# Kernel tuning notes

Measured on AMD Instinct MI355X. Metric: run time of the kernel, lower is better.

The kernel has to match this reference:

```python
import jax, jax.numpy as jnp
import numpy as np

B, H, L, N = 16, 256, 4096, 64
N2 = N // 2  # conjugate-pair parameterization: keep half the state modes


def setup_inputs() -> dict:
    key = jax.random.key(0)
    ks = jax.random.split(key, 12)
    x = jax.random.normal(ks[0], (B, H, L), jnp.float32)
    # BatchNorm1d params + running stats (inference mode)
    g1 = jnp.ones((H,), jnp.float32); b1 = jnp.zeros((H,), jnp.float32)
    m1 = 0.1 * jax.random.normal(ks[1], (H,), jnp.float32)
    v1 = 1.0 + 0.1 * jax.random.uniform(ks[2], (H,), jnp.float32)
    g2 = jnp.ones((H,), jnp.float32); b2 = jnp.zeros((H,), jnp.float32)
    m2 = 0.1 * jax.random.normal(ks[3], (H,), jnp.float32)
    v2 = 1.0 + 0.1 * jax.random.uniform(ks[4], (H,), jnp.float32)
    # S4 SSM kernel parameters (S4D-Lin init); bidirectional -> 2 channels of C
    log_dt = jnp.log(1e-3) + (jnp.log(1e-1) - jnp.log(1e-3)) * jax.random.uniform(ks[5], (H,), jnp.float32)
    logA_re = jnp.log(0.5) * jnp.ones((H, N2), jnp.float32)  # A_real = -exp(logA_re) = -0.5
    A_im = jnp.pi * jnp.broadcast_to(jnp.arange(N2, dtype=jnp.float32), (H, N2))
    C_re = jax.random.normal(ks[6], (2, H, N2), jnp.float32) * np.float32(0.5 ** 0.5)
    C_im = jax.random.normal(ks[7], (2, H, N2), jnp.float32) * np.float32(0.5 ** 0.5)
    D = jax.random.normal(ks[8], (H,), jnp.float32)  # skip term
    # S4 output linear: Conv1d(H, 2H, 1) followed by GLU
    Wo = jax.random.normal(ks[9], (2 * H, H), jnp.float32) / np.float32(np.sqrt(H))
    bo = jnp.zeros((2 * H,), jnp.float32)
    # FFN 1x1 convs
    W2 = jax.random.normal(ks[10], (2 * H, H), jnp.float32) / np.float32(np.sqrt(H))
    b2f = jnp.zeros((2 * H,), jnp.float32)
    W3 = jax.random.normal(ks[11], (H, 2 * H), jnp.float32) / np.float32(np.sqrt(2 * H))
    b3 = jnp.zeros((H,), jnp.float32)
    return dict(x=x, g1=g1, b1=b1, m1=m1, v1=v1, log_dt=log_dt, logA_re=logA_re,
                A_im=A_im, C_re=C_re, C_im=C_im, D=D, Wo=Wo, bo=bo,
                g2=g2, b2=b2, m2=m2, v2=v2, W2=W2, b2f=b2f, W3=W3, b3=b3)


def _bn(x, g, b, m, v, eps=1e-5):
    # inference-mode BatchNorm1d over channel dim of (B, H, L)
    scale = g / jnp.sqrt(v + eps)
    return (x - m[:, None]) * scale[:, None] + b[:, None]


def _s4(x, log_dt, logA_re, A_im, C_re, C_im, D, Wo, bo):
    # x: (B, H, L). Bidirectional diagonal SSM via FFT convolution.
    Ln = x.shape[-1]
    Hh = x.shape[1]
    dt = jnp.exp(log_dt)                               # (H,)
    A = -jnp.exp(logA_re) + 1j * A_im                  # (H, N2)
    dtA = dt[:, None] * A                              # (H, N2)
    C = (C_re + 1j * C_im) * (jnp.exp(dtA) - 1.0) / A  # (2, H, N2) ZOH discretization
    vand = jnp.exp(dtA[:, :, None] * jnp.arange(Ln))   # (H, N2, L) Vandermonde
    k = 2.0 * jnp.einsum('chn,hnl->chl', C, vand).real  # (2, H, L) fwd/bwd kernels
    k_fwd, k_bwd = k[0], k[1]
    zpad = jnp.zeros_like(k_fwd)
    k_full = (jnp.concatenate([k_fwd, zpad], axis=-1)
              + jnp.concatenate([zpad, k_bwd[:, ::-1]], axis=-1))  # (H, 2L)
    u_f = jnp.fft.rfft(x, n=2 * Ln)
    k_f = jnp.fft.rfft(k_full, n=2 * Ln)
    y = jnp.fft.irfft(u_f * k_f, n=2 * Ln)[..., :Ln]   # (B, H, L)
    y = y + D[:, None] * x                             # skip connection
    y = jax.nn.gelu(y, approximate=False)
    z = jnp.einsum('oi,bil->bol', Wo, y) + bo[:, None]  # (B, 2H, L)
    return z[:, :Hh] * jax.nn.sigmoid(z[:, Hh:])        # GLU -> (B, H, L)


def reference(x, g1, b1, m1, v1, log_dt, logA_re, A_im, C_re, C_im, D, Wo, bo,
              g2, b2, m2, v2, W2, b2f, W3, b3):
    # residual 1: BN -> S4 -> add
    res = x
    h = _bn(x, g1, b1, m1, v1)
    h = _s4(h, log_dt, logA_re, A_im, C_re, C_im, D, Wo, bo)
    x = res + h
    # residual 2: BN -> conv1x1(H->2H) -> GELU -> conv1x1(2H->H) -> add
    res = x
    h = _bn(x, g2, b2, m2, v2)
    h = jnp.einsum('oi,bil->bol', W2, h) + b2f[:, None]
    h = jax.nn.gelu(h, approximate=False)
    h = jnp.einsum('oi,bil->bol', W3, h) + b3[:, None]
    return res + h
```

## Files before the change

kernel.cpp:

```cpp
#include <hip/hip_runtime.h>

#define BB 16
#define HH 256
#define LL 4096
#define NN2 32

using f32x16 = __attribute__((ext_vector_type(16))) float;
using bfx8   = __attribute__((ext_vector_type(8))) short;

static constexpr float BN_EPS = 1e-5f;

__device__ __forceinline__ float gelu_exact(float v) {
    return 0.5f * v * (1.0f + erff(v * 0.70710678118654752f));
}
__device__ __forceinline__ float sigmoidf_(float v) {
    return 1.0f / (1.0f + expf(-v));
}
__device__ __forceinline__ ushort f2bf(float f) {
    uint u = __float_as_uint(f);
    u += 0x7fffu + ((u >> 16) & 1u);
    return (ushort)(u >> 16);
}
__device__ __forceinline__ float bf2f(ushort h) {
    return __uint_as_float(((uint)h) << 16);
}
__device__ __forceinline__ int rowstart(int l) {
    return l * 12 + ((l >> 3) & 7) * 4 + ((l >> 6) << 5);
}

__global__ void k_consts(const float* __restrict__ log_dt,
                         const float* __restrict__ logA_re,
                         const float* __restrict__ A_im,
                         const float* __restrict__ C_re,
                         const float* __restrict__ C_im,
                         float* __restrict__ cst) {
    int idx = blockIdx.x * blockDim.x + threadIdx.x;
    if (idx >= HH * NN2) return;
    int h = idx / NN2;
    float dt = expf(log_dt[h]);
    float Ar = -expf(logA_re[idx]);
    float Ai = A_im[idx];
    float er = expf(dt * Ar);
    float wr = er * cosf(dt * Ai);
    float wi = er * sinf(dt * Ai);
    float Er = wr - 1.0f, Ei = wi;
    float inv = 1.0f / (Ar * Ar + Ai * Ai);
    float Fr = (Er * Ar + Ei * Ai) * inv;
    float Fi = (Ei * Ar - Er * Ai) * inv;
    cst[idx] = wr;
    cst[8192 + idx] = wi;
    #pragma unroll
    for (int c = 0; c < 2; ++c) {
        float Cr = C_re[c * HH * NN2 + idx], Ci = C_im[c * HH * NN2 + idx];
        cst[8192 * (2 + 2 * c) + idx] = 2.0f * (Cr * Fr - Ci * Fi);
        cst[8192 * (3 + 2 * c) + idx] = 2.0f * (Cr * Fi + Ci * Fr);
    }
}

__global__ void k_prep2a(const float* __restrict__ g2, const float* __restrict__ b2,
                         const float* __restrict__ m2, const float* __restrict__ v2,
                         float* __restrict__ s2, float* __restrict__ t2) {
    int k = threadIdx.x;
    float s = g2[k] * rsqrtf(v2[k] + BN_EPS);
    s2[k] = s;
    t2[k] = fmaf(-m2[k], s, b2[k]);
}
__global__ void k_prep2b(const float* __restrict__ W2, const float* __restrict__ t2,
                         const float* __restrict__ b2f, float* __restrict__ bias2p) {
    int o = blockIdx.x * 256 + threadIdx.x;
    float acc = b2f[o];
    for (int k = 0; k < 256; ++k) acc = fmaf(W2[o * 256 + k], t2[k], acc);
    bias2p[o] = acc;
}
__global__ void k_wprep(const float* __restrict__ Wo, const float* __restrict__ W2,
                        const float* __restrict__ W3, const float* __restrict__ s2,
                        ushort* __restrict__ WoH, ushort* __restrict__ WoL,
                        ushort* __restrict__ W2H, ushort* __restrict__ W2L,
                        ushort* __restrict__ W3H, ushort* __restrict__ W3L) {
    int i = blockIdx.x * 256 + threadIdx.x;
    int job = i >> 17, e = i & 131071;
    float w; ushort *H, *L;
    if (job == 0)      { w = Wo[e];                  H = WoH; L = WoL; }
    else if (job == 1) { w = W2[e] * s2[e & 255];    H = W2H; L = W2L; }
    else               { w = W3[e];                  H = W3H; L = W3L; }
    ushort h = f2bf(w);
    H[e] = h;
    L[e] = f2bf(w - bf2f(h));
}

__global__ __launch_bounds__(64) void k_scan(const float* __restrict__ x,
                                             const float* __restrict__ g1,
                                             const float* __restrict__ b1,
                                             const float* __restrict__ m1,
                                             const float* __restrict__ v1,
                                             const float* __restrict__ cst,
                                             float* __restrict__ yf,
                                             float* __restrict__ yb) {
    __shared__ float smem[2368];
    int bh = blockIdx.x;
    int h = bh & (HH - 1);
    int lane = threadIdx.x;
    int half = lane >> 5;
    int n = lane & 31;
    int hn = h * NN2 + n;

    float wr = cst[hn];
    float wi = cst[8192 + hn];
    float Cr = cst[8192 * (2 + 2 * half) + hn];
    float Ci = cst[8192 * (3 + 2 * half) + hn];

    float sc = g1[h] * rsqrtf(v1[h] + BN_EPS);
    float sh = fmaf(-m1[h], sc, b1[h]);

    const float* xrow = x + (size_t)bh * LL;
    float* yfr = yf + (size_t)bh * LL;
    float* ybr = yb + (size_t)bh * LL;

    float sr = 0.0f, si = 0.0f;
    const int hbase = half * 1152;
    const int xsw = (n >> 3) << 2;
    const int lbase = hbase + n * 36;
    const int xbase = 2304 + half * 32;

    float xraw = half ? xrow[LL - 1 - n] : xrow[n];

    for (int c = 0; c < LL / 32; ++c) {
        smem[xbase + n] = fmaf(xraw, sc, sh);
        if (c + 1 < LL / 32) {
            int gnext = (c + 1) * 32 + n;
            xraw = half ? xrow[LL - 1 - gnext] : xrow[gnext];
        }
        __syncthreads();

        #pragma unroll
        for (int j = 0; j < 32; j += 4) {
            float4 xq = *(const float4*)&smem[xbase + j];
            float4 cb;
            { float t0 = fmaf(wr, sr, xq.x); float ns = fmaf(wi, sr, wr * si);
              sr = fmaf(-wi, si, t0); si = ns; cb.x = fmaf(Cr, sr, -(Ci * si)); }
            { float t0 = fmaf(wr, sr, xq.y); float ns = fmaf(wi, sr, wr * si);
              sr = fmaf(-wi, si, t0); si = ns; cb.y = fmaf(Cr, sr, -(Ci * si)); }
            { float t0 = fmaf(wr, sr, xq.z); float ns = fmaf(wi, sr, wr * si);
              sr = fmaf(-wi, si, t0); si = ns; cb.z = fmaf(Cr, sr, -(Ci * si)); }
            { float t0 = fmaf(wr, sr, xq.w); float ns = fmaf(wi, sr, wr * si);
              sr = fmaf(-wi, si, t0); si = ns; cb.w = fmaf(Cr, sr, -(Ci * si)); }
            *(float4*)&smem[lbase + (j ^ xsw)] = cb;
        }
        __syncthreads();

        float s0 = 0.0f, s1 = 0.0f, s2 = 0.0f, s3 = 0.0f;
        #pragma unroll
        for (int m = 0; m < 32; m += 4) {
            s0 += smem[hbase + (m + 0) * 36 + (n ^ (((m + 0) >> 3) << 2))];
            s1 += smem[hbase + (m + 1) * 36 + (n ^ (((m + 1) >> 3) << 2))];
            s2 += smem[hbase + (m + 2) * 36 + (n ^ (((m + 2) >> 3) << 2))];
            s3 += smem[hbase + (m + 3) * 36 + (n ^ (((m + 3) >> 3) << 2))];
        }
        float sum = (s0 + s1) + (s2 + s3);
        int gl = c * 32 + n;
        if (half) {
            int oidx = LL - 2 - gl;
            if (oidx >= 0) ybr[oidx] = sum;
        } else {
            yfr[gl] = sum;
        }
    }
}

__global__ void k_combine(const float* __restrict__ x,
                          const float* __restrict__ g1, const float* __restrict__ b1,
                          const float* __restrict__ m1, const float* __restrict__ v1,
                          const float* __restrict__ D,
                          const float* __restrict__ yb, float* __restrict__ y) {
    int i4 = blockIdx.x * blockDim.x + threadIdx.x;
    if (i4 >= BB * HH * LL / 4) return;
    int row = i4 >> 10;
    int h = row & (HH - 1);
    float sc = g1[h] * rsqrtf(v1[h] + BN_EPS);
    float sh = fmaf(-m1[h], sc, b1[h]);
    float d = D[h];
    float4 xv = ((const float4*)x)[i4];
    float4 yv = ((float4*)y)[i4];
    float4 bv = ((const float4*)yb)[i4];
    if ((i4 & 1023) == 1023) bv.w = 0.0f;
    yv.x = gelu_exact(fmaf(d, fmaf(xv.x, sc, sh), yv.x + bv.x));
    yv.y = gelu_exact(fmaf(d, fmaf(xv.y, sc, sh), yv.y + bv.y));
    yv.z = gelu_exact(fmaf(d, fmaf(xv.z, sc, sh), yv.z + bv.z));
    yv.w = gelu_exact(fmaf(d, fmaf(xv.w, sc, sh), yv.w + bv.w));
    ((float4*)y)[i4] = yv;
}

__global__ void k_combine2(const float* __restrict__ x,
                           const float* __restrict__ g1, const float* __restrict__ b1,
                           const float* __restrict__ m1, const float* __restrict__ v1,
                           const float* __restrict__ D,
                           const float* __restrict__ yf, const float* __restrict__ yb,
                           ushort* __restrict__ s4h, ushort* __restrict__ s4l) {
    int i4 = blockIdx.x * blockDim.x + threadIdx.x;
    if (i4 >= BB * HH * LL / 4) return;
    int row = i4 >> 10;
    int h = row & (HH - 1);
    float sc = g1[h] * rsqrtf(v1[h] + BN_EPS);
    float sh = fmaf(-m1[h], sc, b1[h]);
    float d = D[h];
    float4 xv = ((const float4*)x)[i4];
    float4 fv = ((const float4*)yf)[i4];
    float4 bv = ((const float4*)yb)[i4];
    if ((i4 & 1023) == 1023) bv.w = 0.0f;
    float v0 = gelu_exact(fmaf(d, fmaf(xv.x, sc, sh), fv.x + bv.x));
    float v1_ = gelu_exact(fmaf(d, fmaf(xv.y, sc, sh), fv.y + bv.y));
    float v2 = gelu_exact(fmaf(d, fmaf(xv.z, sc, sh), fv.z + bv.z));
    float v3 = gelu_exact(fmaf(d, fmaf(xv.w, sc, sh), fv.w + bv.w));
    ushort4 hh, ll;
    hh.x = f2bf(v0);  ll.x = f2bf(v0 - bf2f(hh.x));
    hh.y = f2bf(v1_); ll.y = f2bf(v1_ - bf2f(hh.y));
    hh.z = f2bf(v2);  ll.z = f2bf(v2 - bf2f(hh.z));
    hh.w = f2bf(v3);  ll.w = f2bf(v3 - bf2f(hh.w));
    ((ushort4*)s4h)[i4] = hh;
    ((ushort4*)s4l)[i4] = ll;
}

template <int MODE>
__global__ __launch_bounds__(256) void k_mgemm(
    const ushort* __restrict__ Ah, const ushort* __restrict__ Al,
    const ushort* __restrict__ Bh, const ushort* __restrict__ Bl,
    const float* __restrict__ bias,
    const float* __restrict__ X,
    float* __restrict__ Outf,
    ushort* __restrict__ Oh, ushort* __restrict__ Ol) {

    constexpr int K  = (MODE == 2) ? 512 : 256;
    constexpr int NK = K / 16;

    __shared__ uint bt[3200];
    __shared__ float gatebuf[(MODE == 0) ? 8192 : 4];

    const int tid  = threadIdx.x;
    const int lane = tid & 63;
    const int w    = tid >> 6;
    const int c31  = lane & 31;
    const int g    = lane >> 5;
    const int gm   = blockIdx.x;
    const int l0   = blockIdx.y * 128;
    const int b    = blockIdx.z;

    int r = w * 32 + c31;
    int arow;
    if (MODE == 0) arow = (r < 64) ? (gm * 64 + r) : (256 + gm * 64 + (r - 64));
    else           arow = gm * 128 + r;
    const ushort* apH = Ah + (size_t)arow * K;
    const ushort* apL = Al + (size_t)arow * K;

    const int pl = tid >> 7;
    const int tt = tid & 127;
    const int kp = tt & 7;
    const int lg = tt >> 3;
    const ushort* bplane = pl ? Bl : Bh;
    const ushort* bbase = bplane + ((size_t)b * K + 2 * kp) * LL + l0 + lg * 8;
    uint* btp = bt + pl * 1600;
    const int wb = 96 * lg + 4 * (lg & 7) + 32 * (lg >> 3);
    const int sl0 = (kp & 3) + 4 * (kp >> 2);
    const int sl1 = (kp & 3) + 4 * ((kp >> 2) ^ 1);

    f32x16 acc[4];
    #pragma unroll
    for (int f = 0; f < 4; ++f)
        #pragma unroll
        for (int e = 0; e < 16; ++e) acc[f][e] = 0.0f;

    uint4 r0 = *(const uint4*)(bbase);
    uint4 r1 = *(const uint4*)(bbase + LL);

    for (int kc = 0; kc < NK; ++kc) {
        __syncthreads();
        {
            uint p0 = (r0.x & 0xffffu) | (r1.x << 16);
            uint p1 = (r0.x >> 16)     | (r1.x & 0xffff0000u);
            uint p2 = (r0.y & 0xffffu) | (r1.y << 16);
            uint p3 = (r0.y >> 16)     | (r1.y & 0xffff0000u);
            uint p4 = (r0.z & 0xffffu) | (r1.z << 16);
            uint p5 = (r0.z >> 16)     | (r1.z & 0xffff0000u);
            uint p6 = (r0.w & 0xffffu) | (r1.w << 16);
            uint p7 = (r0.w >> 16)     | (r1.w & 0xffff0000u);
            btp[wb +  0 + sl0] = p0;
            btp[wb + 12 + sl1] = p1;
            btp[wb + 24 + sl0] = p2;
            btp[wb + 36 + sl1] = p3;
            btp[wb + 48 + sl0] = p4;
            btp[wb + 60 + sl1] = p5;
            btp[wb + 72 + sl0] = p6;
            btp[wb + 84 + sl1] = p7;
        }
        __syncthreads();
        if (kc + 1 < NK) {
            const ushort* nb = bbase + (size_t)((kc + 1) * 16) * LL;
            r0 = *(const uint4*)(nb);
            r1 = *(const uint4*)(nb + LL);
        }
        bfx8 ah = *(const bfx8*)(apH + kc * 16 + 8 * g);
        bfx8 al = *(const bfx8*)(apL + kc * 16 + 8 * g);
        #pragma unroll
        for (int f = 0; f < 4; ++f) {
            int l = f * 32 + c31;
            int ra = rowstart(l) + ((g ^ (l & 1)) << 2);
            bfx8 bhf = *(const bfx8*)(bt + ra);
            bfx8 blf = *(const bfx8*)(bt + 1600 + ra);
            acc[f] = __builtin_amdgcn_mfma_f32_32x32x16_bf16(ah, bhf, acc[f], 0, 0, 0);
            acc[f] = __builtin_amdgcn_mfma_f32_32x32x16_bf16(ah, blf, acc[f], 0, 0, 0);
            acc[f] = __builtin_amdgcn_mfma_f32_32x32x16_bf16(al, bhf, acc[f], 0, 0, 0);
        }
    }

    if (MODE == 0) {
        if (w >= 2) {
            int grow_base = (w - 2) * 32;
            int og_base = 256 + gm * 64 + grow_base;
            #pragma unroll
            for (int f = 0; f < 4; ++f)
                #pragma unroll
                for (int reg = 0; reg < 16; ++reg) {
                    int rr = (reg & 3) + 8 * (reg >> 2) + 4 * g;
                    float zg = acc[f][reg] + bias[og_base + rr];
                    gatebuf[(grow_base + rr) * 128 + f * 32 + c31] = sigmoidf_(zg);
                }
        }
        __syncthreads();
        if (w < 2) {
            int vr_base = w * 32;
            #pragma unroll
            for (int f = 0; f < 4; ++f)
                #pragma unroll
                for (int reg = 0; reg < 16; ++reg) {
                    int rr = (reg & 3) + 8 * (reg >> 2) + 4 * g;
                    int vr = vr_base + rr;
                    int ov = gm * 64 + vr;
                    size_t oi = ((size_t)b * HH + ov) * LL + l0 + f * 32 + c31;
                    float zv = acc[f][reg] + bias[ov];
                    float res = X[oi] + zv * gatebuf[vr * 128 + f * 32 + c31];
                    Outf[oi] = res;
                    ushort hh = f2bf(res);
                    Oh[oi] = hh;
                    Ol[oi] = f2bf(res - bf2f(hh));
                }
        }
    } else if (MODE == 1) {
        #pragma unroll
        for (int f = 0; f < 4; ++f)
            #pragma unroll
            for (int reg = 0; reg < 16; ++reg) {
                int rr = (reg & 3) + 8 * (reg >> 2) + 4 * g;
                int o = gm * 128 + w * 32 + rr;
                size_t oi = ((size_t)b * 512 + o) * LL + l0 + f * 32 + c31;
                float v = gelu_exact(acc[f][reg] + bias[o]);
                ushort hh = f2bf(v);
                Oh[oi] = hh;
                Ol[oi] = f2bf(v - bf2f(hh));
            }
    } else {
        #pragma unroll
        for (int f = 0; f < 4; ++f)
            #pragma unroll
            for (int reg = 0; reg < 16; ++reg) {
                int rr = (reg & 3) + 8 * (reg >> 2) + 4 * g;
                int o = gm * 128 + w * 32 + rr;
                size_t oi = ((size_t)b * HH + o) * LL + l0 + f * 32 + c31;
                Outf[oi] = Outf[oi] + acc[f][reg] + bias[o];
            }
    }
}

template <int MODE>
__global__ __launch_bounds__(256) void k_gemm(const float* __restrict__ A,
                                              const float* __restrict__ Bm,
                                              const float* __restrict__ bias,
                                              const float* __restrict__ X,
                                              const float* __restrict__ bng,
                                              const float* __restrict__ bnb,
                                              const float* __restrict__ bnm,
                                              const float* __restrict__ bnv,
                                              float* __restrict__ Out) {
    constexpr int K  = (MODE == 2) ? 512 : 256;
    constexpr int CH = (MODE == 2) ? 512 : 256;
    constexpr int OC = (MODE == 1) ? 512 : 256;

    __shared__ float As[32][128];
    __shared__ float Bs[32][64];

    int tid = threadIdx.x;
    int tx = tid & 15, ty = tid >> 4;
    int gm = blockIdx.x;
    int l0 = blockIdx.y * 64;
    int b  = blockIdx.z;

    int lm = tid & 127;
    int kg = (tid >> 7) << 4;
    int grow;
    if (MODE == 0) grow = (lm < 64) ? (gm * 64 + lm) : (256 + gm * 64 + (lm - 64));
    else           grow = gm * 128 + lm;
    const float* arow = A + (size_t)grow * K + kg;

    int bl = (tid & 15) * 4;
    int bk = tid >> 4;

    float acc[2][4][4] = {};

    for (int k0 = 0; k0 < K; k0 += 32) {
        float4 av[4];
        #pragma unroll
        for (int t = 0; t < 4; ++t) av[t] = *(const float4*)(arow + k0 + t * 4);

        const float* brow0 = Bm + ((size_t)b * CH + k0 + bk) * LL + l0 + bl;
        float4 bv0 = *(const float4*)brow0;
        float4 bv1 = *(const float4*)(brow0 + (size_t)16 * LL);
        if (MODE == 1) {
            int i0 = k0 + bk, i1 = i0 + 16;
            float s0 = bng[i0] * rsqrtf(bnv[i0] + BN_EPS);
            float h0 = fmaf(-bnm[i0], s0, bnb[i0]);
            float s1 = bng[i1] * rsqrtf(bnv[i1] + BN_EPS);
            float h1 = fmaf(-bnm[i1], s1, bnb[i1]);
            bv0.x = fmaf(bv0.x, s0, h0); bv0.y = fmaf(bv0.y, s0, h0);
            bv0.z = fmaf(bv0.z, s0, h0); bv0.w = fmaf(bv0.w, s0, h0);
            bv1.x = fmaf(bv1.x, s1, h1); bv1.y = fmaf(bv1.y, s1, h1);
            bv1.z = fmaf(bv1.z, s1, h1); bv1.w = fmaf(bv1.w, s1, h1);
        }

        __syncthreads();
        #pragma unroll
        for (int t = 0; t < 4; ++t) {
            As[kg + t * 4 + 0][lm] = av[t].x;
            As[kg + t * 4 + 1][lm] = av[t].y;
            As[kg + t * 4 + 2][lm] = av[t].z;
            As[kg + t * 4 + 3][lm] = av[t].w;
        }
        *(float4*)&Bs[bk][bl]      = bv0;
        *(float4*)&Bs[bk + 16][bl] = bv1;
        __syncthreads();

        #pragma unroll
        for (int kk = 0; kk < 32; ++kk) {
            float4 a0 = *(const float4*)&As[kk][ty * 4];
            float4 a1 = *(const float4*)&As[kk][64 + ty * 4];
            float4 bq = *(const float4*)&Bs[kk][tx * 4];
            float a0v[4] = {a0.x, a0.y, a0.z, a0.w};
            float a1v[4] = {a1.x, a1.y, a1.z, a1.w};
            float bqv[4] = {bq.x, bq.y, bq.z, bq.w};
            #pragma unroll
            for (int rr = 0; rr < 4; ++rr)
                #pragma unroll
                for (int cc = 0; cc < 4; ++cc) {
                    acc[0][rr][cc] = fmaf(a0v[rr], bqv[cc], acc[0][rr][cc]);
                    acc[1][rr][cc] = fmaf(a1v[rr], bqv[cc], acc[1][rr][cc]);
                }
        }
    }

    #pragma unroll
    for (int rr = 0; rr < 4; ++rr) {
        if (MODE == 0) {
            int o1 = gm * 64 + ty * 4 + rr;
            size_t oi = ((size_t)b * OC + o1) * LL + l0 + tx * 4;
            float bz1 = bias[o1], bz2 = bias[o1 + 256];
            float4 xr = *(const float4*)(X + oi);
            float4 rv;
            rv.x = xr.x + (acc[0][rr][0] + bz1) * sigmoidf_(acc[1][rr][0] + bz2);
            rv.y = xr.y + (acc[0][rr][1] + bz1) * sigmoidf_(acc[1][rr][1] + bz2);
            rv.z = xr.z + (acc[0][rr][2] + bz1) * sigmoidf_(acc[1][rr][2] + bz2);
            rv.w = xr.w + (acc[0][rr][3] + bz1) * sigmoidf_(acc[1][rr][3] + bz2);
            *(float4*)(Out + oi) = rv;
        } else if (MODE == 1) {
            int o0 = gm * 128 + ty * 4 + rr;
            #pragma unroll
            for (int hf = 0; hf < 2; ++hf) {
                int o = o0 + hf * 64;
                size_t oi = ((size_t)b * OC + o) * LL + l0 + tx * 4;
                float bz = bias[o];
                float4 rv;
                rv.x = gelu_exact(acc[hf][rr][0] + bz);
                rv.y = gelu_exact(acc[hf][rr][1] + bz);
                rv.z = gelu_exact(acc[hf][rr][2] + bz);
                rv.w = gelu_exact(acc[hf][rr][3] + bz);
                *(float4*)(Out + oi) = rv;
            }
        } else {
            int o0 = gm * 128 + ty * 4 + rr;
            #pragma unroll
            for (int hf = 0; hf < 2; ++hf) {
                int o = o0 + hf * 64;
                size_t oi = ((size_t)b * OC + o) * LL + l0 + tx * 4;
                float bz = bias[o];
                float4 xr = *(const float4*)(X + oi);
                float4 rv;
                rv.x = xr.x + acc[hf][rr][0] + bz;
                rv.y = xr.y + acc[hf][rr][1] + bz;
                rv.z = xr.z + acc[hf][rr][2] + bz;
                rv.w = xr.w + acc[hf][rr][3] + bz;
                *(float4*)(Out + oi) = rv;
            }
        }
    }
}

extern "C" void kernel_launch(void* const* d_in, const int* in_sizes, int n_in,
                              void* d_out, int out_size, void* d_ws, size_t ws_size,
                              hipStream_t stream) {
    const float* x       = (const float*)d_in[0];
    const float* g1      = (const float*)d_in[1];
    const float* b1      = (const float*)d_in[2];
    const float* m1      = (const float*)d_in[3];
    const float* v1      = (const float*)d_in[4];
    const float* log_dt  = (const float*)d_in[5];
    const float* logA_re = (const float*)d_in[6];
    const float* A_im    = (const float*)d_in[7];
    const float* C_re    = (const float*)d_in[8];
    const float* C_im    = (const float*)d_in[9];
    const float* D       = (const float*)d_in[10];
    const float* Wo      = (const float*)d_in[11];
    const float* bo      = (const float*)d_in[12];
    const float* g2      = (const float*)d_in[13];
    const float* b2      = (const float*)d_in[14];
    const float* m2      = (const float*)d_in[15];
    const float* v2      = (const float*)d_in[16];
    const float* W2      = (const float*)d_in[17];
    const float* b2f     = (const float*)d_in[18];
    const float* W3      = (const float*)d_in[19];
    const float* b3      = (const float*)d_in[20];
    float* out = (float*)d_out;
    char* wsb = (char*)d_ws;

    const size_t MB = 1024 * 1024;
    const size_t NEEDED = 194 * MB;

    if (ws_size >= NEEDED) {
        float*  cst    = (float*)wsb;
        float*  s2     = (float*)(wsb + 196608);
        float*  t2     = (float*)(wsb + 197632);
        float*  bias2p = (float*)(wsb + 198656);
        ushort* WoH = (ushort*)(wsb + 262144);
        ushort* WoL = (ushort*)(wsb + 524288);
        ushort* W2H = (ushort*)(wsb + 786432);
        ushort* W2L = (ushort*)(wsb + 1048576);
        ushort* W3H = (ushort*)(wsb + 1310720);
        ushort* W3L = (ushort*)(wsb + 1572864);
        float*  yf  = (float*)(wsb + 2 * MB);
        float*  yb  = (float*)(wsb + 66 * MB);
        ushort* s4h = (ushort*)(wsb + 130 * MB);
        ushort* s4l = (ushort*)(wsb + 162 * MB);
        ushort* x1h = (ushort*)(wsb + 2 * MB);
        ushort* x1l = (ushort*)(wsb + 34 * MB);
        ushort* h2h = (ushort*)(wsb + 66 * MB);
        ushort* h2l = (ushort*)(wsb + 130 * MB);

        k_consts<<<dim3(HH * NN2 / 256), dim3(256), 0, stream>>>(log_dt, logA_re, A_im, C_re, C_im, cst);
        k_prep2a<<<dim3(1), dim3(256), 0, stream>>>(g2, b2, m2, v2, s2, t2);
        k_wprep<<<dim3(1536), dim3(256), 0, stream>>>(Wo, W2, W3, s2, WoH, WoL, W2H, W2L, W3H, W3L);
        k_prep2b<<<dim3(2), dim3(256), 0, stream>>>(W2, t2, b2f, bias2p);
        k_scan<<<dim3(BB * HH), dim3(64), 0, stream>>>(x, g1, b1, m1, v1, cst, yf, yb);
        k_combine2<<<dim3(BB * HH * LL / 4 / 256), dim3(256), 0, stream>>>(x, g1, b1, m1, v1, D, yf, yb, s4h, s4l);
        k_mgemm<0><<<dim3(4, 32, 16), dim3(256), 0, stream>>>(WoH, WoL, s4h, s4l, bo, x, out, x1h, x1l);
        k_mgemm<1><<<dim3(4, 32, 16), dim3(256), 0, stream>>>(W2H, W2L, x1h, x1l, bias2p, nullptr, nullptr, h2h, h2l);
        k_mgemm<2><<<dim3(2, 32, 16), dim3(256), 0, stream>>>(W3H, W3L, h2h, h2l, b3, nullptr, out, nullptr, nullptr);
    } else {
        float* yf  = (float*)wsb;
        float* yb  = (float*)(wsb + 64 * MB);
        float* h2  = (float*)wsb;
        float* cst = (float*)(wsb + 128 * MB);

        k_consts<<<dim3(HH * NN2 / 256), dim3(256), 0, stream>>>(log_dt, logA_re, A_im, C_re, C_im, cst);
        k_scan<<<dim3(BB * HH), dim3(64), 0, stream>>>(x, g1, b1, m1, v1, cst, yf, yb);
        k_combine<<<dim3(BB * HH * LL / 4 / 256), dim3(256), 0, stream>>>(x, g1, b1, m1, v1, D, yb, yf);
        k_gemm<0><<<dim3(4, 64, 16), dim3(256), 0, stream>>>(Wo, yf, bo, x,
                                                             nullptr, nullptr, nullptr, nullptr, out);
        k_gemm<1><<<dim3(4, 64, 16), dim3(256), 0, stream>>>(W2, out, b2f, nullptr,
                                                             g2, b2, m2, v2, h2);
        k_gemm<2><<<dim3(2, 64, 16), dim3(256), 0, stream>>>(W3, h2, b3, out,
                                                             nullptr, nullptr, nullptr, nullptr, out);
    }
}
```

Baseline: 982.1 us.

## Store scan and activation intermediates in single bf16, drop low-part planes

Scan outputs and GEMM activation intermediates are now stored as single bf16 values instead of fp32 or bf16 hi+lo pairs. The activation low-part MFMA is removed, leaving two MFMAs per step instead of three, and the B-staging shared memory is halved. The scan now loads x with register-double-buffered float4 loads rather than staging it through shared memory. The fp32 fallback path is removed. Together these cut memory traffic and MFMA work, at the cost of lower activation precision, which may affect tolerance.

Measured after the change: 902.7 us. 1.09x faster.

```diff
diff --git a/kernel.cpp b/kernel.cpp
--- a/kernel.cpp
+++ b/kernel.cpp
@@ -94,9 +94,9 @@
                                              const float* __restrict__ m1,
                                              const float* __restrict__ v1,
                                              const float* __restrict__ cst,
-                                             float* __restrict__ yf,
-                                             float* __restrict__ yb) {
-    __shared__ float smem[2368];
+                                             ushort* __restrict__ yf,
+                                             ushort* __restrict__ yb) {
+    __shared__ float smem[2304];
     int bh = blockIdx.x;
     int h = bh & (HH - 1);
     int lane = threadIdx.x;
@@ -113,38 +113,49 @@
     float sh = fmaf(-m1[h], sc, b1[h]);
 
     const float* xrow = x + (size_t)bh * LL;
-    float* yfr = yf + (size_t)bh * LL;
-    float* ybr = yb + (size_t)bh * LL;
+    ushort* yfr = yf + (size_t)bh * LL;
+    ushort* ybr = yb + (size_t)bh * LL;
 
     float sr = 0.0f, si = 0.0f;
     const int hbase = half * 1152;
     const int xsw = (n >> 3) << 2;
     const int lbase = hbase + n * 36;
-    const int xbase = 2304 + half * 32;
-
-    float xraw = half ? xrow[LL - 1 - n] : xrow[n];
-
-    for (int c = 0; c < LL / 32; ++c) {
-        smem[xbase + n] = fmaf(xraw, sc, sh);
+
+    auto ldx = [&](int c, int t) -> float4 {
+        return half ? *(const float4*)(xrow + LL - 4 - c * 32 - 4 * t)
+                    : *(const float4*)(xrow + c * 32 + 4 * t);
+    };
+
+    float4 bufA[8], bufB[8];
+    #pragma unroll
+    for (int t = 0; t < 8; ++t) bufA[t] = ldx(0, t);
+
+    auto step = [&](float4 (&cur)[8], float4 (&nxt)[8], int c) {
         if (c + 1 < LL / 32) {
-            int gnext = (c + 1) * 32 + n;
-            xraw = half ? xrow[LL - 1 - gnext] : xrow[gnext];
-        }
-        __syncthreads();
-
-        #pragma unroll
-        for (int j = 0; j < 32; j += 4) {
-            float4 xq = *(const float4*)&smem[xbase + j];
+            #pragma unroll
+            for (int t = 0; t < 8; ++t) nxt[t] = ldx(c + 1, t);
+        }
+        #pragma unroll
+        for (int t = 0; t < 8; ++t) {
+            float4 f = cur[t];
+            float v0 = half ? f.w : f.x;
+            float v1_ = half ? f.z : f.y;
+            float v2 = half ? f.y : f.z;
+            float v3 = half ? f.x : f.w;
             float4 cb;
-            { float t0 = fmaf(wr, sr, xq.x); float ns = fmaf(wi, sr, wr * si);
+            { float xv = fmaf(v0, sc, sh);
+              float t0 = fmaf(wr, sr, xv); float ns = fmaf(wi, sr, wr * si);
               sr = fmaf(-wi, si, t0); si = ns; cb.x = fmaf(Cr, sr, -(Ci * si)); }
-            { float t0 = fmaf(wr, sr, xq.y); float ns = fmaf(wi, sr, wr * si);
+            { float xv = fmaf(v1_, sc, sh);
+              float t0 = fmaf(wr, sr, xv); float ns = fmaf(wi, sr, wr * si);
               sr = fmaf(-wi, si, t0); si = ns; cb.y = fmaf(Cr, sr, -(Ci * si)); }
-            { float t0 = fmaf(wr, sr, xq.z); float ns = fmaf(wi, sr, wr * si);
+            { float xv = fmaf(v2, sc, sh);
+              float t0 = fmaf(wr, sr, xv); float ns = fmaf(wi, sr, wr * si);
               sr = fmaf(-wi, si, t0); si = ns; cb.z = fmaf(Cr, sr, -(Ci * si)); }
-            { float t0 = fmaf(wr, sr, xq.w); float ns = fmaf(wi, sr, wr * si);
+            { float xv = fmaf(v3, sc, sh);
+              float t0 = fmaf(wr, sr, xv); float ns = fmaf(wi, sr, wr * si);
               sr = fmaf(-wi, si, t0); si = ns; cb.w = fmaf(Cr, sr, -(Ci * si)); }
-            *(float4*)&smem[lbase + (j ^ xsw)] = cb;
+            *(float4*)&smem[lbase + ((4 * t) ^ xsw)] = cb;
         }
         __syncthreads();
 
@@ -160,18 +171,25 @@
         int gl = c * 32 + n;
         if (half) {
             int oidx = LL - 2 - gl;
-            if (oidx >= 0) ybr[oidx] = sum;
+            if (oidx >= 0) ybr[oidx] = f2bf(sum);
         } else {
-            yfr[gl] = sum;
-        }
+            yfr[gl] = f2bf(sum);
+        }
+        __syncthreads();
+    };
+
+    for (int c = 0; c < LL / 32; c += 2) {
+        step(bufA, bufB, c);
+        step(bufB, bufA, c + 1);
     }
 }
 
-__global__ void k_combine(const float* __restrict__ x,
-                          const float* __restrict__ g1, const float* __restrict__ b1,
-                          const float* __restrict__ m1, const float* __restrict__ v1,
-                          const float* __restrict__ D,
-                          const float* __restrict__ yb, float* __restrict__ y) {
+__global__ void k_combine2(const float* __restrict__ x,
+                           const float* __restrict__ g1, const float* __restrict__ b1,
+                           const float* __restrict__ m1, const float* __restrict__ v1,
+                           const float* __restrict__ D,
+                           const ushort* __restrict__ yf, const ushort* __restrict__ yb,
+                           ushort* __restrict__ s4h) {
     int i4 = blockIdx.x * blockDim.x + threadIdx.x;
     if (i4 >= BB * HH * LL / 4) return;
     int row = i4 >> 10;
@@ -180,59 +198,31 @@
     float sh = fmaf(-m1[h], sc, b1[h]);
     float d = D[h];
     float4 xv = ((const float4*)x)[i4];
-    float4 yv = ((float4*)y)[i4];
-    float4 bv = ((const float4*)yb)[i4];
-    if ((i4 & 1023) == 1023) bv.w = 0.0f;
-    yv.x = gelu_exact(fmaf(d, fmaf(xv.x, sc, sh), yv.x + bv.x));
-    yv.y = gelu_exact(fmaf(d, fmaf(xv.y, sc, sh), yv.y + bv.y));
-    yv.z = gelu_exact(fmaf(d, fmaf(xv.z, sc, sh), yv.z + bv.z));
-    yv.w = gelu_exact(fmaf(d, fmaf(xv.w, sc, sh), yv.w + bv.w));
-    ((float4*)y)[i4] = yv;
-}
-
-__global__ void k_combine2(const float* __restrict__ x,
-                           const float* __restrict__ g1, const float* __restrict__ b1,
-                           const float* __restrict__ m1, const float* __restrict__ v1,
-                           const float* __restrict__ D,
-                           const float* __restrict__ yf, const float* __restrict__ yb,
-                           ushort* __restrict__ s4h, ushort* __restrict__ s4l) {
-    int i4 = blockIdx.x * blockDim.x + threadIdx.x;
-    if (i4 >= BB * HH * LL / 4) return;
-    int row = i4 >> 10;
-    int h = row & (HH - 1);
-    float sc = g1[h] * rsqrtf(v1[h] + BN_EPS);
-    float sh = fmaf(-m1[h], sc, b1[h]);
-    float d = D[h];
-    float4 xv = ((const float4*)x)[i4];
-    float4 fv = ((const float4*)yf)[i4];
-    float4 bv = ((const float4*)yb)[i4];
-    if ((i4 & 1023) == 1023) bv.w = 0.0f;
-    float v0 = gelu_exact(fmaf(d, fmaf(xv.x, sc, sh), fv.x + bv.x));
-    float v1_ = gelu_exact(fmaf(d, fmaf(xv.y, sc, sh), fv.y + bv.y));
-    float v2 = gelu_exact(fmaf(d, fmaf(xv.z, sc, sh), fv.z + bv.z));
-    float v3 = gelu_exact(fmaf(d, fmaf(xv.w, sc, sh), fv.w + bv.w));
-    ushort4 hh, ll;
-    hh.x = f2bf(v0);  ll.x = f2bf(v0 - bf2f(hh.x));
-    hh.y = f2bf(v1_); ll.y = f2bf(v1_ - bf2f(hh.y));
-    hh.z = f2bf(v2);  ll.z = f2bf(v2 - bf2f(hh.z));
-    hh.w = f2bf(v3);  ll.w = f2bf(v3 - bf2f(hh.w));
+    ushort4 fu = ((const ushort4*)yf)[i4];
+    ushort4 bu = ((const ushort4*)yb)[i4];
+    if ((i4 & 1023) == 1023) bu.w = 0;
+    float v0 = gelu_exact(fmaf(d, fmaf(xv.x, sc, sh), bf2f(fu.x) + bf2f(bu.x)));
+    float v1_ = gelu_exact(fmaf(d, fmaf(xv.y, sc, sh), bf2f(fu.y) + bf2f(bu.y)));
+    float v2 = gelu_exact(fmaf(d, fmaf(xv.z, sc, sh), bf2f(fu.z) + bf2f(bu.z)));
+    float v3 = gelu_exact(fmaf(d, fmaf(xv.w, sc, sh), bf2f(fu.w) + bf2f(bu.w)));
+    ushort4 hh;
+    hh.x = f2bf(v0); hh.y = f2bf(v1_); hh.z = f2bf(v2); hh.w = f2bf(v3);
     ((ushort4*)s4h)[i4] = hh;
-    ((ushort4*)s4l)[i4] = ll;
 }
 
 template <int MODE>
 __global__ __launch_bounds__(256) void k_mgemm(
     const ushort* __restrict__ Ah, const ushort* __restrict__ Al,
-    const ushort* __restrict__ Bh, const ushort* __restrict__ Bl,
+    const ushort* __restrict__ Bh,
     const float* __restrict__ bias,
     const float* __restrict__ X,
     float* __restrict__ Outf,
-    ushort* __restrict__ Oh, ushort* __restrict__ Ol) {
+    ushort* __restrict__ Oh) {
 
     constexpr int K  = (MODE == 2) ? 512 : 256;
     constexpr int NK = K / 16;
 
-    __shared__ uint bt[3200];
+    __shared__ uint bt[1600];
     __shared__ float gatebuf[(MODE == 0) ? 8192 : 4];
 
     const int tid  = threadIdx.x;
@@ -251,13 +241,12 @@
     const ushort* apH = Ah + (size_t)arow * K;
     const ushort* apL = Al + (size_t)arow * K;
 
-    const int pl = tid >> 7;
     const int tt = tid & 127;
+    const int hi = tid >> 7;
     const int kp = tt & 7;
     const int lg = tt >> 3;
-    const ushort* bplane = pl ? Bl : Bh;
-    const ushort* bbase = bplane + ((size_t)b * K + 2 * kp) * LL + l0 + lg * 8;
-    uint* btp = bt + pl * 1600;
+    const int j0 = hi * 4;
+    const ushort* bbase = Bh + ((size_t)b * K + 2 * kp) * LL + l0 + lg * 8 + hi * 4;
     const int wb = 96 * lg + 4 * (lg & 7) + 32 * (lg >> 3);
     const int sl0 = (kp & 3) + 4 * (kp >> 2);
     const int sl1 = (kp & 3) + 4 * ((kp >> 2) ^ 1);
@@ -268,8 +257,8 @@
         #pragma unroll
         for (int e = 0; e < 16; ++e) acc[f][e] = 0.0f;
 
-    uint4 r0 = *(const uint4*)(bbase);
-    uint4 r1 = *(const uint4*)(bbase + LL);
+    uint2 r0 = *(const uint2*)(bbase);
+    uint2 r1 = *(const uint2*)(bbase + LL);
 
     for (int kc = 0; kc < NK; ++kc) {
         __syncthreads();
@@ -278,24 +267,16 @@
             uint p1 = (r0.x >> 16)     | (r1.x & 0xffff0000u);
             uint p2 = (r0.y & 0xffffu) | (r1.y << 16);
             uint p3 = (r0.y >> 16)     | (r1.y & 0xffff0000u);
-            uint p4 = (r0.z & 0xffffu) | (r1.z << 16);
-            uint p5 = (r0.z >> 16)     | (r1.z & 0xffff0000u);
-            uint p6 = (r0.w & 0xffffu) | (r1.w << 16);
-            uint p7 = (r0.w >> 16)     | (r1.w & 0xffff0000u);
-            btp[wb +  0 + sl0] = p0;
-            btp[wb + 12 + sl1] = p1;
-            btp[wb + 24 + sl0] = p2;
-            btp[wb + 36 + sl1] = p3;
-            btp[wb + 48 + sl0] = p4;
-            btp[wb + 60 + sl1] = p5;
-            btp[wb + 72 + sl0] = p6;
-            btp[wb + 84 + sl1] = p7;
+            bt[wb + 12 * (j0 + 0) + sl0] = p0;
+            bt[wb + 12 * (j0 + 1) + sl1] = p1;
+            bt[wb + 12 * (j0 + 2) + sl0] = p2;
+            bt[wb + 12 * (j0 + 3) + sl1] = p3;
         }
         __syncthreads();
         if (kc + 1 < NK) {
             const ushort* nb = bbase + (size_t)((kc + 1) * 16) * LL;
-            r0 = *(const uint4*)(nb);
-            r1 = *(const uint4*)(nb + LL);
+            r0 = *(const uint2*)(nb);
+            r1 = *(const uint2*)(nb + LL);
         }
         bfx8 ah = *(const bfx8*)(apH + kc * 16 + 8 * g);
         bfx8 al = *(const bfx8*)(apL + kc * 16 + 8 * g);
@@ -304,9 +285,7 @@
             int l = f * 32 + c31;
             int ra = rowstart(l) + ((g ^ (l & 1)) << 2);
             bfx8 bhf = *(const bfx8*)(bt + ra);
-            bfx8 blf = *(const bfx8*)(bt + 1600 + ra);
             acc[f] = __builtin_amdgcn_mfma_f32_32x32x16_bf16(ah, bhf, acc[f], 0, 0, 0);
-            acc[f] = __builtin_amdgcn_mfma_f32_32x32x16_bf16(ah, blf, acc[f], 0, 0, 0);
             acc[f] = __builtin_amdgcn_mfma_f32_32x32x16_bf16(al, bhf, acc[f], 0, 0, 0);
         }
     }
@@ -338,9 +317,7 @@
                     float zv = acc[f][reg] + bias[ov];
                     float res = X[oi] + zv * gatebuf[vr * 128 + f * 32 + c31];
                     Outf[oi] = res;
-                    ushort hh = f2bf(res);
-                    Oh[oi] = hh;
-                    Ol[oi] = f2bf(res - bf2f(hh));
+                    Oh[oi] = f2bf(res);
                 }
         }
     } else if (MODE == 1) {
@@ -352,9 +329,7 @@
                 int o = gm * 128 + w * 32 + rr;
                 size_t oi = ((size_t)b * 512 + o) * LL + l0 + f * 32 + c31;
                 float v = gelu_exact(acc[f][reg] + bias[o]);
-                ushort hh = f2bf(v);
-                Oh[oi] = hh;
-                Ol[oi] = f2bf(v - bf2f(hh));
+                Oh[oi] = f2bf(v);
             }
     } else {
         #pragma unroll
@@ -366,137 +341,6 @@
                 size_t oi = ((size_t)b * HH + o) * LL + l0 + f * 32 + c31;
                 Outf[oi] = Outf[oi] + acc[f][reg] + bias[o];
             }
-    }
-}
-
-template <int MODE>
-__global__ __launch_bounds__(256) void k_gemm(const float* __restrict__ A,
-                                              const float* __restrict__ Bm,
-                                              const float* __restrict__ bias,
-                                              const float* __restrict__ X,
-                                              const float* __restrict__ bng,
-                                              const float* __restrict__ bnb,
-                                              const float* __restrict__ bnm,
-                                              const float* __restrict__ bnv,
-                                              float* __restrict__ Out) {
-    constexpr int K  = (MODE == 2) ? 512 : 256;
-    constexpr int CH = (MODE == 2) ? 512 : 256;
-    constexpr int OC = (MODE == 1) ? 512 : 256;
-
-    __shared__ float As[32][128];
-    __shared__ float Bs[32][64];
-
-    int tid = threadIdx.x;
-    int tx = tid & 15, ty = tid >> 4;
-    int gm = blockIdx.x;
-    int l0 = blockIdx.y * 64;
-    int b  = blockIdx.z;
-
-    int lm = tid & 127;
-    int kg = (tid >> 7) << 4;
-    int grow;
-    if (MODE == 0) grow = (lm < 64) ? (gm * 64 + lm) : (256 + gm * 64 + (lm - 64));
-    else           grow = gm * 128 + lm;
-    const float* arow = A + (size_t)grow * K + kg;
-
-    int bl = (tid & 15) * 4;
-    int bk = tid >> 4;
-
-    float acc[2][4][4] = {};
-
-    for (int k0 = 0; k0 < K; k0 += 32) {
-        float4 av[4];
-        #pragma unroll
-        for (int t = 0; t < 4; ++t) av[t] = *(const float4*)(arow + k0 + t * 4);
-
-        const float* brow0 = Bm + ((size_t)b * CH + k0 + bk) * LL + l0 + bl;
-        float4 bv0 = *(const float4*)brow0;
-        float4 bv1 = *(const float4*)(brow0 + (size_t)16 * LL);
-        if (MODE == 1) {
-            int i0 = k0 + bk, i1 = i0 + 16;
-            float s0 = bng[i0] * rsqrtf(bnv[i0] + BN_EPS);
-            float h0 = fmaf(-bnm[i0], s0, bnb[i0]);
-            float s1 = bng[i1] * rsqrtf(bnv[i1] + BN_EPS);
-            float h1 = fmaf(-bnm[i1], s1, bnb[i1]);
-            bv0.x = fmaf(bv0.x, s0, h0); bv0.y = fmaf(bv0.y, s0, h0);
-            bv0.z = fmaf(bv0.z, s0, h0); bv0.w = fmaf(bv0.w, s0, h0);
-            bv1.x = fmaf(bv1.x, s1, h1); bv1.y = fmaf(bv1.y, s1, h1);
-            bv1.z = fmaf(bv1.z, s1, h1); bv1.w = fmaf(bv1.w, s1, h1);
-        }
-
-        __syncthreads();
-        #pragma unroll
-        for (int t = 0; t < 4; ++t) {
-            As[kg + t * 4 + 0][lm] = av[t].x;
-            As[kg + t * 4 + 1][lm] = av[t].y;
-            As[kg + t * 4 + 2][lm] = av[t].z;
-            As[kg + t * 4 + 3][lm] = av[t].w;
-        }
-        *(float4*)&Bs[bk][bl]      = bv0;
-        *(float4*)&Bs[bk + 16][bl] = bv1;
-        __syncthreads();
-
-        #pragma unroll
-        for (int kk = 0; kk < 32; ++kk) {
-            float4 a0 = *(const float4*)&As[kk][ty * 4];
-            float4 a1 = *(const float4*)&As[kk][64 + ty * 4];
-            float4 bq = *(const float4*)&Bs[kk][tx * 4];
-            float a0v[4] = {a0.x, a0.y, a0.z, a0.w};
-            float a1v[4] = {a1.x, a1.y, a1.z, a1.w};
-            float bqv[4] = {bq.x, bq.y, bq.z, bq.w};
-            #pragma unroll
-            for (int rr = 0; rr < 4; ++rr)
-                #pragma unroll
-                for (int cc = 0; cc < 4; ++cc) {
-                    acc[0][rr][cc] = fmaf(a0v[rr], bqv[cc], acc[0][rr][cc]);
-                    acc[1][rr][cc] = fmaf(a1v[rr], bqv[cc], acc[1][rr][cc]);
-                }
-        }
-    }
-
-    #pragma unroll
-    for (int rr = 0; rr < 4; ++rr) {
-        if (MODE == 0) {
-            int o1 = gm * 64 + ty * 4 + rr;
-            size_t oi = ((size_t)b * OC + o1) * LL + l0 + tx * 4;
-            float bz1 = bias[o1], bz2 = bias[o1 + 256];
-            float4 xr = *(const float4*)(X + oi);
-            float4 rv;
-            rv.x = xr.x + (acc[0][rr][0] + bz1) * sigmoidf_(acc[1][rr][0] + bz2);
-            rv.y = xr.y + (acc[0][rr][1] + bz1) * sigmoidf_(acc[1][rr][1] + bz2);
-            rv.z = xr.z + (acc[0][rr][2] + bz1) * sigmoidf_(acc[1][rr][2] + bz2);
-            rv.w = xr.w + (acc[0][rr][3] + bz1) * sigmoidf_(acc[1][rr][3] + bz2);
-            *(float4*)(Out + oi) = rv;
-        } else if (MODE == 1) {
-            int o0 = gm * 128 + ty * 4 + rr;
-            #pragma unroll
-            for (int hf = 0; hf < 2; ++hf) {
-                int o = o0 + hf * 64;
-                size_t oi = ((size_t)b * OC + o) * LL + l0 + tx * 4;
-                float bz = bias[o];
-                float4 rv;
-                rv.x = gelu_exact(acc[hf][rr][0] + bz);
-                rv.y = gelu_exact(acc[hf][rr][1] + bz);
-                rv.z = gelu_exact(acc[hf][rr][2] + bz);
-                rv.w = gelu_exact(acc[hf][rr][3] + bz);
-                *(float4*)(Out + oi) = rv;
-            }
-        } else {
-            int o0 = gm * 128 + ty * 4 + rr;
-            #pragma unroll
-            for (int hf = 0; hf < 2; ++hf) {
-                int o = o0 + hf * 64;
-                size_t oi = ((size_t)b * OC + o) * LL + l0 + tx * 4;
-                float bz = bias[o];
-                float4 xr = *(const float4*)(X + oi);
-                float4 rv;
-                rv.x = xr.x + acc[hf][rr][0] + bz;
-                rv.y = xr.y + acc[hf][rr][1] + bz;
-                rv.z = xr.z + acc[hf][rr][2] + bz;
-                rv.w = xr.w + acc[hf][rr][3] + bz;
-                *(float4*)(Out + oi) = rv;
-            }
-        }
     }
 }
 
@@ -528,51 +372,30 @@
     char* wsb = (char*)d_ws;
 
     const size_t MB = 1024 * 1024;
-    const size_t NEEDED = 194 * MB;
-
-    if (ws_size >= NEEDED) {
-        float*  cst    = (float*)wsb;
-        float*  s2     = (float*)(wsb + 196608);
-        float*  t2     = (float*)(wsb + 197632);
-        float*  bias2p = (float*)(wsb + 198656);
-        ushort* WoH = (ushort*)(wsb + 262144);
-        ushort* WoL = (ushort*)(wsb + 524288);
-        ushort* W2H = (ushort*)(wsb + 786432);
-        ushort* W2L = (ushort*)(wsb + 1048576);
-        ushort* W3H = (ushort*)(wsb + 1310720);
-        ushort* W3L = (ushort*)(wsb + 1572864);
-        float*  yf  = (float*)(wsb + 2 * MB);
-        float*  yb  = (float*)(wsb + 66 * MB);
-        ushort* s4h = (ushort*)(wsb + 130 * MB);
-        ushort* s4l = (ushort*)(wsb + 162 * MB);
-        ushort* x1h = (ushort*)(wsb + 2 * MB);
-        ushort* x1l = (ushort*)(wsb + 34 * MB);
-        ushort* h2h = (ushort*)(wsb + 66 * MB);
-        ushort* h2l = (ushort*)(wsb + 130 * MB);
-
-        k_consts<<<dim3(HH * NN2 / 256), dim3(256), 0, stream>>>(log_dt, logA_re, A_im, C_re, C_im, cst);
-        k_prep2a<<<dim3(1), dim3(256), 0, stream>>>(g2, b2, m2, v2, s2, t2);
-        k_wprep<<<dim3(1536), dim3(256), 0, stream>>>(Wo, W2, W3, s2, WoH, WoL, W2H, W2L, W3H, W3L);
-        k_prep2b<<<dim3(2), dim3(256), 0, stream>>>(W2, t2, b2f, bias2p);
-        k_scan<<<dim3(BB * HH), dim3(64), 0, stream>>>(x, g1, b1, m1, v1, cst, yf, yb);
-        k_combine2<<<dim3(BB * HH * LL / 4 / 256), dim3(256), 0, stream>>>(x, g1, b1, m1, v1, D, yf, yb, s4h, s4l);
-        k_mgemm<0><<<dim3(4, 32, 16), dim3(256), 0, stream>>>(WoH, WoL, s4h, s4l, bo, x, out, x1h, x1l);
-        k_mgemm<1><<<dim3(4, 32, 16), dim3(256), 0, stream>>>(W2H, W2L, x1h, x1l, bias2p, nullptr, nullptr, h2h, h2l);
-        k_mgemm<2><<<dim3(2, 32, 16), dim3(256), 0, stream>>>(W3H, W3L, h2h, h2l, b3, nullptr, out, nullptr, nullptr);
-    } else {
-        float* yf  = (float*)wsb;
-        float* yb  = (float*)(wsb + 64 * MB);
-        float* h2  = (float*)wsb;
-        float* cst = (float*)(wsb + 128 * MB);
-
-        k_consts<<<dim3(HH * NN2 / 256), dim3(256), 0, stream>>>(log_dt, logA_re, A_im, C_re, C_im, cst);
-        k_scan<<<dim3(BB * HH), dim3(64), 0, stream>>>(x, g1, b1, m1, v1, cst, yf, yb);
-        k_combine<<<dim3(BB * HH * LL / 4 / 256), dim3(256), 0, stream>>>(x, g1, b1, m1, v1, D, yb, yf);
-        k_gemm<0><<<dim3(4, 64, 16), dim3(256), 0, stream>>>(Wo, yf, bo, x,
-                                                             nullptr, nullptr, nullptr, nullptr, out);
-        k_gemm<1><<<dim3(4, 64, 16), dim3(256), 0, stream>>>(W2, out, b2f, nullptr,
-                                                             g2, b2, m2, v2, h2);
-        k_gemm<2><<<dim3(2, 64, 16), dim3(256), 0, stream>>>(W3, h2, b3, out,
-                                                             nullptr, nullptr, nullptr, nullptr, out);
-    }
-}
+
+    float*  cst    = (float*)wsb;
+    float*  s2     = (float*)(wsb + 196608);
+    float*  t2     = (float*)(wsb + 197632);
+    float*  bias2p = (float*)(wsb + 198656);
+    ushort* WoH = (ushort*)(wsb + 262144);
+    ushort* WoL = (ushort*)(wsb + 524288);
+    ushort* W2H = (ushort*)(wsb + 786432);
+    ushort* W2L = (ushort*)(wsb + 1048576);
+    ushort* W3H = (ushort*)(wsb + 1310720);
+    ushort* W3L = (ushort*)(wsb + 1572864);
+    ushort* yf  = (ushort*)(wsb + 2 * MB);
+    ushort* yb  = (ushort*)(wsb + 34 * MB);
+    ushort* s4h = (ushort*)(wsb + 66 * MB);
+    ushort* x1h = (ushort*)(wsb + 98 * MB);
+    ushort* h2h = (ushort*)(wsb + 130 * MB);
+
+    k_consts<<<dim3(HH * NN2 / 256), dim3(256), 0, stream>>>(log_dt, logA_re, A_im, C_re, C_im, cst);
+    k_prep2a<<<dim3(1), dim3(256), 0, stream>>>(g2, b2, m2, v2, s2, t2);
+    k_wprep<<<dim3(1536), dim3(256), 0, stream>>>(Wo, W2, W3, s2, WoH, WoL, W2H, W2L, W3H, W3L);
+    k_prep2b<<<dim3(2), dim3(256), 0, stream>>>(W2, t2, b2f, bias2p);
+    k_scan<<<dim3(BB * HH), dim3(64), 0, stream>>>(x, g1, b1, m1, v1, cst, yf, yb);
+    k_combine2<<<dim3(BB * HH * LL / 4 / 256), dim3(256), 0, stream>>>(x, g1, b1, m1, v1, D, yf, yb, s4h);
+    k_mgemm<0><<<dim3(4, 32, 16), dim3(256), 0, stream>>>(WoH, WoL, s4h, bo, x, out, x1h);
+    k_mgemm<1><<<dim3(4, 32, 16), dim3(256), 0, stream>>>(W2H, W2L, x1h, bias2p, nullptr, nullptr, h2h);
+    k_mgemm<2><<<dim3(2, 32, 16), dim3(256), 0, stream>>>(W3H, W3L, h2h, b3, nullptr, out, nullptr);
+}
```
